# Performance work log

Measured on AMD Instinct MI355X. Metric: run time of the kernel, lower is better.

The kernel has to match this reference:

```python
import jax, jax.numpy as jnp
import numpy as np

NEG_SLOPE = 0.01  # torch LeakyReLU default

def setup_inputs() -> dict:
    key = jax.random.key(0)
    ks = jax.random.split(key, 8)
    B, T, D = 8, 2048, 512
    E, H = 8, 2 * D  # n_experts, ffn hidden
    s = 0.02
    return {
        "x":  jax.random.normal(ks[0], (B, T, D), dtype=jnp.float32),
        "Wr": jax.random.normal(ks[1], (D, E), dtype=jnp.float32) * s,
        "br": jnp.zeros((E,), dtype=jnp.float32),
        "W1": jax.random.normal(ks[2], (E, D, H), dtype=jnp.float32) * s,
        "b1": jnp.zeros((E, H), dtype=jnp.float32),
        "W2": jax.random.normal(ks[3], (E, H, D), dtype=jnp.float32) * s,
        "b2": jnp.zeros((E, D), dtype=jnp.float32),
    }

def reference(x, Wr, br, W1, b1, W2, b2):
    B, T, D = x.shape
    E = Wr.shape[1]
    top_k = 2
    balancing_coef = 1e-4
    x_flat = x.reshape(B * T, D)  # [N, D]

    # router: softmax over experts
    router_probs = jax.nn.softmax(x_flat @ Wr + br, axis=-1)  # [N, E]
    top_weights, top_indices = jax.lax.top_k(router_probs, top_k)  # [N, k]

    # dense all-expert FFN (faithful to original: every expert on every token)
    h = jax.nn.leaky_relu(jnp.einsum('nd,edh->neh', x_flat, W1) + b1, NEG_SLOPE)  # [N, E, H]
    expert_out = jax.nn.leaky_relu(jnp.einsum('neh,ehd->ned', h, W2) + b2, NEG_SLOPE)  # [N, E, D]
    # dropout is identity in eval mode

    # gather top-k expert outputs and combine with router weights
    top_out = jnp.take_along_axis(expert_out, top_indices[:, :, None], axis=1)  # [N, k, D]
    out_flat = jnp.sum(top_out * top_weights[:, :, None], axis=1)  # [N, D]
    output = out_flat.reshape(B, T, D)

    # load-balancing loss
    target = jnp.full((E,), 1.0 / E, dtype=x.dtype)
    mean_probs = jnp.mean(router_probs, axis=0)
    gating_loss = jnp.mean((target - mean_probs) ** 2) * balancing_coef
    return (output, gating_loss)
```

## Files before the change

### kernel.cpp

```cpp
#include <hip/hip_runtime.h>
#include <hip/hip_bf16.h>

constexpr int D_    = 512;
constexpr int H_    = 1024;
constexpr int E_    = 8;
constexpr int NTOK_ = 16384;
constexpr int MT_   = 64;
constexpr int NPAIR_= 2*NTOK_;
constexpr float NEG_ = 0.01f;

typedef short s16x8 __attribute__((ext_vector_type(8)));
typedef float f32x4 __attribute__((ext_vector_type(4)));

#define MFMA16(a,b,c) __builtin_amdgcn_mfma_f32_16x16x32_bf16((a),(b),(c),0,0,0)

__device__ __forceinline__ unsigned short f2bf(float f) {
  unsigned u = __float_as_uint(f);
  u += 0x7FFFu + ((u >> 16) & 1u);
  return (unsigned short)(u >> 16);
}
__device__ __forceinline__ float bf2f(unsigned u16) {
  return __uint_as_float(u16 << 16);
}
__device__ __forceinline__ float leaky(float v) {
  return v > 0.f ? v : NEG_ * v;
}

__global__ __launch_bounds__(256) void prep_kernel(
    const float* __restrict__ x, const float* __restrict__ Wr,
    const float* __restrict__ br,
    const float* __restrict__ W1, const float* __restrict__ W2,
    unsigned short* __restrict__ W1s, unsigned short* __restrict__ W2s,
    int* __restrict__ cnt, float* __restrict__ psum,
    int* __restrict__ tokE, int* __restrict__ tokSlot, float* __restrict__ tokW) {
  const int blk = blockIdx.x;
  const int tid = threadIdx.x;
  if (blk < 64) {
    __shared__ int lcnt[E_];
    __shared__ int gbase[E_];
    __shared__ float lp[E_];
    if (tid < E_) { lcnt[tid] = 0; lp[tid] = 0.f; }
    __syncthreads();

    int t = blk * 256 + tid;
    float acc[E_];
#pragma unroll
    for (int e = 0; e < E_; e++) acc[e] = br[e];
    const float4* xr = (const float4*)(x + (size_t)t * D_);
    for (int i = 0; i < D_ / 4; i++) {
      float4 v = xr[i];
      const float* w = Wr + (size_t)i * 4 * E_;
#pragma unroll
      for (int e = 0; e < E_; e++)
        acc[e] += v.x * w[e] + v.y * w[8 + e] + v.z * w[16 + e] + v.w * w[24 + e];
    }
    float mx = acc[0];
#pragma unroll
    for (int e = 1; e < E_; e++) mx = fmaxf(mx, acc[e]);
    float p[E_]; float s = 0.f;
#pragma unroll
    for (int e = 0; e < E_; e++) { p[e] = expf(acc[e] - mx); s += p[e]; }
    float inv = 1.f / s;
#pragma unroll
    for (int e = 0; e < E_; e++) p[e] *= inv;

    float m1 = -1.f, m2 = -1.f; int i1 = 0, i2 = 0;
#pragma unroll
    for (int e = 0; e < E_; e++) {
      float pe = p[e];
      if (pe > m1)      { m2 = m1; i2 = i1; m1 = pe; i1 = e; }
      else if (pe > m2) { m2 = pe; i2 = e; }
    }
    int s1 = atomicAdd(&lcnt[i1], 1);
    int s2 = atomicAdd(&lcnt[i2], 1);

#pragma unroll
    for (int e = 0; e < E_; e++) {
      float v = p[e];
#pragma unroll
      for (int o = 32; o > 0; o >>= 1) v += __shfl_xor(v, o);
      if ((tid & 63) == 0) atomicAdd(&lp[e], v);
    }
    __syncthreads();
    if (tid < E_) {
      gbase[tid] = atomicAdd(&cnt[tid * 16], lcnt[tid]);
      atomicAdd(&psum[tid * 16], lp[tid]);
    }
    __syncthreads();
    tokE[2 * t]     = i1; tokSlot[2 * t]     = gbase[i1] + s1; tokW[2 * t]     = m1;
    tokE[2 * t + 1] = i2; tokSlot[2 * t + 1] = gbase[i2] + s2; tokW[2 * t + 1] = m2;
  } else {
    __shared__ float ldsf[64][68];
    int bid = blk - 64;
    const float* src;
    int e, kt, tc, srcStride;
    bool isW1 = bid < 1024;
    if (isW1) {
      e = bid >> 7; kt = (bid >> 4) & 7; tc = bid & 15; srcStride = 1024;
      src = W1 + ((size_t)(e * 512 + kt * 64)) * 1024 + tc * 64;
    } else {
      int b2 = bid - 1024;
      e = b2 >> 7; kt = (b2 >> 3) & 15; tc = b2 & 7; srcStride = 512;
      src = W2 + ((size_t)(e * 1024 + kt * 64)) * 512 + tc * 64;
    }
#pragma unroll
    for (int rep = 0; rep < 4; rep++) {
      int row = rep * 16 + (tid >> 4);
      int c4  = (tid & 15) * 4;
      float4 v = *(const float4*)(src + (size_t)row * srcStride + c4);
      ldsf[row][c4] = v.x; ldsf[row][c4 + 1] = v.y;
      ldsf[row][c4 + 2] = v.z; ldsf[row][c4 + 3] = v.w;
    }
    __syncthreads();
    int wv = tid >> 6, lane = tid & 63;
#pragma unroll
    for (int qi = 0; qi < 2; qi++) {
      int q = wv * 2 + qi;
      int ks = q >> 2, nt = q & 3;
      int k0 = ks * 32 + (lane >> 4) * 8;
      int n  = nt * 16 + (lane & 15);
      s16x8 v;
#pragma unroll
      for (int j = 0; j < 8; j++) v[j] = (short)f2bf(ldsf[k0 + j][n]);
      if (isW1) {
        int ntg = tc * 4 + nt, kkg = kt * 2 + ks;
        *(s16x8*)(W1s + (((size_t)e << 16) + (ntg << 10) + (kkg << 6) + lane) * 8) = v;
      } else {
        int ntg = tc * 4 + nt, kkg = kt * 2 + ks;
        *(s16x8*)(W2s + (((size_t)e << 16) + (ntg << 11) + (kkg << 6) + lane) * 8) = v;
      }
    }
  }
}

__global__ __launch_bounds__(256) void assign_kernel(
    const int* __restrict__ tokE, const int* __restrict__ tokSlot,
    const int* __restrict__ cnt, const float* __restrict__ psum,
    int* __restrict__ posOfTok, int* __restrict__ tokOfPos,
    float* __restrict__ loss_out) {
  __shared__ int soff[E_];
  int tid = threadIdx.x;
  if (tid == 0) {
    int o = 0;
#pragma unroll
    for (int e = 0; e < E_; e++) { soff[e] = o; o += cnt[e * 16]; }
  }
  __syncthreads();
  int p = blockIdx.x * 256 + tid;
  int pos = soff[tokE[p]] + tokSlot[p];
  posOfTok[p] = pos;
  tokOfPos[pos] = p >> 1;
  if (blockIdx.x == 0 && tid == 0) {
    float l = 0.f;
#pragma unroll
    for (int e = 0; e < E_; e++) {
      float d = 0.125f - psum[e * 16] / (float)NTOK_;
      l += d * d;
    }
    *loss_out = (l / 8.f) * 1e-4f;
  }
}

__global__ __launch_bounds__(512, 2) void ffn_kernel(
    const float* __restrict__ x,
    const unsigned short* __restrict__ W1s, const unsigned short* __restrict__ W2s,
    const float* __restrict__ b1, const float* __restrict__ b2,
    const int* __restrict__ cnt, const int* __restrict__ tokOfPos,
    unsigned short* __restrict__ buf) {
  const int e = blockIdx.x & 7;
  const int tile = blockIdx.x >> 3;
  int nTok = 0, base0 = 0;
#pragma unroll
  for (int i = 0; i < E_; i++) {
    int ci = cnt[i * 16];
    if (i < e) base0 += ci;
    if (i == e) nTok = ci;
  }
  const int start = tile * MT_;
  if (start >= nTok) return;
  const int valid = min(MT_, nTok - start);
  const int base = base0 + start;

  __shared__ __align__(16) unsigned short xs[MT_][D_ + 8];
  __shared__ __align__(16) unsigned short hs[MT_][D_ + 8];

  const int tid = threadIdx.x;
  const int w = tid >> 6;
  const int lane = tid & 63;

  for (int r = w; r < MT_; r += 8) {
    int tok = tokOfPos[base + min(r, valid - 1)];
    const float4* src = (const float4*)(x + (size_t)tok * D_);
    float4 a = src[lane * 2], b = src[lane * 2 + 1];
    s16x8 v;
    v[0] = (short)f2bf(a.x); v[1] = (short)f2bf(a.y);
    v[2] = (short)f2bf(a.z); v[3] = (short)f2bf(a.w);
    v[4] = (short)f2bf(b.x); v[5] = (short)f2bf(b.y);
    v[6] = (short)f2bf(b.z); v[7] = (short)f2bf(b.w);
    *(s16x8*)&xs[r][lane * 8] = v;
  }
  __syncthreads();

  const int qm = lane & 15;
  const int qk = (lane >> 4) * 8;
  const int qr = (lane >> 4) * 4;

  f32x4 acc2[4][4];
#pragma unroll
  for (int mi = 0; mi < 4; mi++)
#pragma unroll
    for (int ni = 0; ni < 4; ni++) acc2[mi][ni] = {0.f, 0.f, 0.f, 0.f};

  const unsigned short* B1w = W1s + ((size_t)(e * 64 + w * 4) * 16) * 512 + lane * 8;
  const unsigned short* B2w = W2s + ((size_t)(e * 32 + w * 4) * 32) * 512 + lane * 8;

  for (int c = 0; c < 2; c++) {
    f32x4 acc1[4][4];
#pragma unroll
    for (int mi = 0; mi < 4; mi++)
#pragma unroll
      for (int ni = 0; ni < 4; ni++) acc1[mi][ni] = {0.f, 0.f, 0.f, 0.f};

    const unsigned short* B1c = B1w + (size_t)(c * 32 * 16) * 512;
    float bb[4];
#pragma unroll
    for (int ni = 0; ni < 4; ni++)
      bb[ni] = b1[e * H_ + c * 512 + w * 64 + ni * 16 + qm];

    s16x8 bfp[2][4], afp[2][4];
#pragma unroll
    for (int s = 0; s < 2; s++) {
#pragma unroll
      for (int ni = 0; ni < 4; ni++)
        bfp[s][ni] = *(const s16x8*)(B1c + (size_t)(ni * 16 + s) * 512);
#pragma unroll
      for (int mi = 0; mi < 4; mi++)
        afp[s][mi] = *(const s16x8*)&xs[mi * 16 + qm][s * 32 + qk];
    }
#pragma unroll
    for (int kk = 0; kk < 16; kk++) {
      s16x8 bcur[4], acur[4];
#pragma unroll
      for (int ni = 0; ni < 4; ni++) bcur[ni] = bfp[kk & 1][ni];
#pragma unroll
      for (int mi = 0; mi < 4; mi++) acur[mi] = afp[kk & 1][mi];
      if (kk + 2 < 16) {
#pragma unroll
        for (int ni = 0; ni < 4; ni++)
          bfp[kk & 1][ni] = *(const s16x8*)(B1c + (size_t)(ni * 16 + kk + 2) * 512);
#pragma unroll
        for (int mi = 0; mi < 4; mi++)
          afp[kk & 1][mi] = *(const s16x8*)&xs[mi * 16 + qm][(kk + 2) * 32 + qk];
      }
#pragma unroll
      for (int ni = 0; ni < 4; ni++)
#pragma unroll
        for (int mi = 0; mi < 4; mi++)
          acc1[mi][ni] = MFMA16(acur[mi], bcur[ni], acc1[mi][ni]);
    }
    __syncthreads();

    const unsigned short* B2c = B2w + (size_t)(c * 16) * 512;
    s16x8 b2p[2][4];
#pragma unroll
    for (int s = 0; s < 2; s++)
#pragma unroll
      for (int ni = 0; ni < 4; ni++)
        b2p[s][ni] = *(const s16x8*)(B2c + (size_t)(ni * 32 + s) * 512);

#pragma unroll
    for (int ni = 0; ni < 4; ni++) {
      int hcol = w * 64 + ni * 16 + qm;
#pragma unroll
      for (int mi = 0; mi < 4; mi++)
#pragma unroll
        for (int r4 = 0; r4 < 4; r4++)
          hs[mi * 16 + qr + r4][hcol] = f2bf(leaky(acc1[mi][ni][r4] + bb[ni]));
    }
    __syncthreads();

    s16x8 a2p[2][4];
#pragma unroll
    for (int s = 0; s < 2; s++)
#pragma unroll
      for (int mi = 0; mi < 4; mi++)
        a2p[s][mi] = *(const s16x8*)&hs[mi * 16 + qm][s * 32 + qk];
#pragma unroll
    for (int kk = 0; kk < 16; kk++) {
      s16x8 bcur[4], acur[4];
#pragma unroll
      for (int ni = 0; ni < 4; ni++) bcur[ni] = b2p[kk & 1][ni];
#pragma unroll
      for (int mi = 0; mi < 4; mi++) acur[mi] = a2p[kk & 1][mi];
      if (kk + 2 < 16) {
#pragma unroll
        for (int ni = 0; ni < 4; ni++)
          b2p[kk & 1][ni] = *(const s16x8*)(B2c + (size_t)(ni * 32 + kk + 2) * 512);
#pragma unroll
        for (int mi = 0; mi < 4; mi++)
          a2p[kk & 1][mi] = *(const s16x8*)&hs[mi * 16 + qm][(kk + 2) * 32 + qk];
      }
#pragma unroll
      for (int ni = 0; ni < 4; ni++)
#pragma unroll
        for (int mi = 0; mi < 4; mi++)
          acc2[mi][ni] = MFMA16(acur[mi], bcur[ni], acc2[mi][ni]);
    }
  }

#pragma unroll
  for (int mi = 0; mi < 4; mi++) {
#pragma unroll
    for (int r4 = 0; r4 < 4; r4++) {
      int row = mi * 16 + qr + r4;
      if (row < valid) {
        size_t rowbase = (size_t)(base + row) * D_;
#pragma unroll
        for (int ni = 0; ni < 4; ni++) {
          int col = w * 64 + ni * 16 + qm;
          float v = leaky(acc2[mi][ni][r4] + b2[e * D_ + col]);
          buf[rowbase + col] = f2bf(v);
        }
      }
    }
  }
}

__global__ __launch_bounds__(256) void combine_kernel(
    const unsigned short* __restrict__ buf, const int* __restrict__ posOfTok,
    const float* __restrict__ tokW, float* __restrict__ out) {
  int t = blockIdx.x * 4 + (threadIdx.x >> 6);
  int lane = threadIdx.x & 63;
  int p0 = posOfTok[2 * t], p1 = posOfTok[2 * t + 1];
  float w0 = tokW[2 * t], w1 = tokW[2 * t + 1];
  uint4 u0 = ((const uint4*)(buf + (size_t)p0 * D_))[lane];
  uint4 u1 = ((const uint4*)(buf + (size_t)p1 * D_))[lane];
  float4 oA, oB;
  oA.x = w0 * bf2f(u0.x & 0xFFFFu) + w1 * bf2f(u1.x & 0xFFFFu);
  oA.y = w0 * bf2f(u0.x >> 16)     + w1 * bf2f(u1.x >> 16);
  oA.z = w0 * bf2f(u0.y & 0xFFFFu) + w1 * bf2f(u1.y & 0xFFFFu);
  oA.w = w0 * bf2f(u0.y >> 16)     + w1 * bf2f(u1.y >> 16);
  oB.x = w0 * bf2f(u0.z & 0xFFFFu) + w1 * bf2f(u1.z & 0xFFFFu);
  oB.y = w0 * bf2f(u0.z >> 16)     + w1 * bf2f(u1.z >> 16);
  oB.z = w0 * bf2f(u0.w & 0xFFFFu) + w1 * bf2f(u1.w & 0xFFFFu);
  oB.w = w0 * bf2f(u0.w >> 16)     + w1 * bf2f(u1.w >> 16);
  float4* dst = (float4*)(out + (size_t)t * D_);
  dst[lane * 2]     = oA;
  dst[lane * 2 + 1] = oB;
}

extern "C" void kernel_launch(void* const* d_in, const int* in_sizes, int n_in,
                              void* d_out, int out_size, void* d_ws, size_t ws_size,
                              hipStream_t stream) {
  const float* x  = (const float*)d_in[0];
  const float* Wr = (const float*)d_in[1];
  const float* br = (const float*)d_in[2];
  const float* W1 = (const float*)d_in[3];
  const float* b1 = (const float*)d_in[4];
  const float* W2 = (const float*)d_in[5];
  const float* b2 = (const float*)d_in[6];
  float* out = (float*)d_out;

  char* ws = (char*)d_ws;
  int*   cnt      = (int*)(ws + 0);
  float* psum     = (float*)(ws + 512);
  int*   tokE     = (int*)(ws + 4096);
  int*   tokSlot  = (int*)(ws + 4096 + 1 * 131072);
  float* tokW     = (float*)(ws + 4096 + 2 * 131072);
  int*   posOfTok = (int*)(ws + 4096 + 3 * 131072);
  int*   tokOfPos = (int*)(ws + 4096 + 4 * 131072);
  unsigned short* W1s = (unsigned short*)(ws + (1u << 20));
  unsigned short* W2s = (unsigned short*)(ws + (1u << 20) + 16777216u);
  unsigned short* buf = (unsigned short*)(ws + (1u << 20) + 33554432u);

  hipMemsetAsync(d_ws, 0, 2048, stream);
  prep_kernel<<<64 + 2048, 256, 0, stream>>>(x, Wr, br, W1, W2, W1s, W2s,
                                             cnt, psum, tokE, tokSlot, tokW);
  assign_kernel<<<NPAIR_ / 256, 256, 0, stream>>>(tokE, tokSlot, cnt, psum,
                                                  posOfTok, tokOfPos,
                                                  out + (size_t)NTOK_ * D_);
  ffn_kernel<<<(NTOK_ / MT_) * E_, 512, 0, stream>>>(x, W1s, W2s, b1, b2,
                                                     cnt, tokOfPos, buf);
  combine_kernel<<<NTOK_ / 4, 256, 0, stream>>>(buf, posOfTok, tokW, out);
}
```

Baseline: 295.1 us.

## Fuse router, weight prep, FFN and combine into one cooperative persistent kernel

Replaces the four separate kernel launches with a single cooperative kernel of 256 blocks that uses grid-wide syncs between the routing/weight-conversion, assignment, expert FFN and combine phases. The router is recomputed with LDS-staged x and Wr, eight lanes per token, and the FFN loop becomes persistent over virtual tiles. A per-wave rotation of the K index is added to spread weight-fragment loads across waves. The aim is to remove launch gaps and tail effects, at the cost of grid-sync overhead, a fixed grid of 256 blocks, and 148 KB of shared memory per block, which limits occupancy to one block per CU despite the launch bound hint.

```diff
diff --git a/kernel.cpp b/kernel.cpp
--- a/kernel.cpp
+++ b/kernel.cpp
@@ -1,12 +1,14 @@
 #include <hip/hip_runtime.h>
 #include <hip/hip_bf16.h>
+#include <hip/hip_cooperative_groups.h>
+
+namespace cg = cooperative_groups;
 
 constexpr int D_    = 512;
 constexpr int H_    = 1024;
 constexpr int E_    = 8;
 constexpr int NTOK_ = 16384;
 constexpr int MT_   = 64;
-constexpr int NPAIR_= 2*NTOK_;
 constexpr float NEG_ = 0.01f;
 
 typedef short s16x8 __attribute__((ext_vector_type(8)));
@@ -26,360 +28,372 @@
   return v > 0.f ? v : NEG_ * v;
 }
 
-__global__ __launch_bounds__(256) void prep_kernel(
-    const float* __restrict__ x, const float* __restrict__ Wr,
-    const float* __restrict__ br,
-    const float* __restrict__ W1, const float* __restrict__ W2,
-    unsigned short* __restrict__ W1s, unsigned short* __restrict__ W2s,
-    int* __restrict__ cnt, float* __restrict__ psum,
-    int* __restrict__ tokE, int* __restrict__ tokSlot, float* __restrict__ tokW) {
-  const int blk = blockIdx.x;
-  const int tid = threadIdx.x;
-  if (blk < 64) {
-    __shared__ int lcnt[E_];
-    __shared__ int gbase[E_];
-    __shared__ float lp[E_];
+struct Params {
+  const float *x, *Wr, *br, *W1, *bias1, *W2, *bias2;
+  unsigned short *W1s, *W2s;
+  int *cnt; float *psum;
+  int *tokE, *tokSlot; float *tokW;
+  int *posOfTok, *tokOfPos;
+  unsigned short *buf;
+  float *out, *loss_out;
+};
+
+__global__ __launch_bounds__(512, 2) void fused_kernel(Params P) {
+  __shared__ __align__(16) char smem[148608];
+  cg::grid_group grid = cg::this_grid();
+  const int tid  = threadIdx.x;
+  const int w    = tid >> 6;
+  const int lane = tid & 63;
+  const int blk  = blockIdx.x;
+
+  {
+    float (*xl)[516] = (float (*)[516])smem;
+    float* wrl  = (float*)(smem + 132096);
+    int*   lcnt = (int*)(smem + 148480);
+    int*   gb   = (int*)(smem + 148512);
+    float* lp   = (float*)(smem + 148544);
     if (tid < E_) { lcnt[tid] = 0; lp[tid] = 0.f; }
+    {
+      const float4* s4 = (const float4*)P.Wr;
+      float4* d4 = (float4*)wrl;
+      d4[tid * 2] = s4[tid * 2]; d4[tid * 2 + 1] = s4[tid * 2 + 1];
+    }
+    const int t0 = blk * 64;
+    for (int r2 = 0; r2 < 8; r2++) {
+      int row = w * 8 + r2;
+      const float4* src = (const float4*)(P.x + (size_t)(t0 + row) * D_);
+      float4 a = src[lane * 2], b = src[lane * 2 + 1];
+      *(float4*)&xl[row][lane * 8] = a;
+      *(float4*)&xl[row][lane * 8 + 4] = b;
+    }
     __syncthreads();
-
-    int t = blk * 256 + tid;
-    float acc[E_];
-#pragma unroll
-    for (int e = 0; e < E_; e++) acc[e] = br[e];
-    const float4* xr = (const float4*)(x + (size_t)t * D_);
-    for (int i = 0; i < D_ / 4; i++) {
-      float4 v = xr[i];
-      const float* w = Wr + (size_t)i * 4 * E_;
-#pragma unroll
-      for (int e = 0; e < E_; e++)
-        acc[e] += v.x * w[e] + v.y * w[8 + e] + v.z * w[16 + e] + v.w * w[24 + e];
-    }
-    float mx = acc[0];
-#pragma unroll
-    for (int e = 1; e < E_; e++) mx = fmaxf(mx, acc[e]);
-    float p[E_]; float s = 0.f;
-#pragma unroll
-    for (int e = 0; e < E_; e++) { p[e] = expf(acc[e] - mx); s += p[e]; }
+    const int tg = lane >> 3, eg = lane & 7;
+    const int tokl = w * 8 + tg;
+    float acc = P.br[eg];
+    for (int d = 0; d < D_; d += 4) {
+      float4 xv = *(const float4*)&xl[tokl][d];
+      acc += xv.x * wrl[d * 8 + eg] + xv.y * wrl[d * 8 + 8 + eg] +
+             xv.z * wrl[d * 8 + 16 + eg] + xv.w * wrl[d * 8 + 24 + eg];
+    }
+    float lg[8];
+#pragma unroll
+    for (int e = 0; e < 8; e++) lg[e] = __shfl(acc, (lane & 56) | e);
+    float mx = lg[0];
+#pragma unroll
+    for (int e = 1; e < 8; e++) mx = fmaxf(mx, lg[e]);
+    float p[8], s = 0.f;
+#pragma unroll
+    for (int e = 0; e < 8; e++) { p[e] = expf(lg[e] - mx); s += p[e]; }
     float inv = 1.f / s;
 #pragma unroll
-    for (int e = 0; e < E_; e++) p[e] *= inv;
-
+    for (int e = 0; e < 8; e++) p[e] *= inv;
     float m1 = -1.f, m2 = -1.f; int i1 = 0, i2 = 0;
 #pragma unroll
-    for (int e = 0; e < E_; e++) {
+    for (int e = 0; e < 8; e++) {
       float pe = p[e];
       if (pe > m1)      { m2 = m1; i2 = i1; m1 = pe; i1 = e; }
       else if (pe > m2) { m2 = pe; i2 = e; }
     }
-    int s1 = atomicAdd(&lcnt[i1], 1);
-    int s2 = atomicAdd(&lcnt[i2], 1);
-
-#pragma unroll
-    for (int e = 0; e < E_; e++) {
-      float v = p[e];
-#pragma unroll
-      for (int o = 32; o > 0; o >>= 1) v += __shfl_xor(v, o);
-      if ((tid & 63) == 0) atomicAdd(&lp[e], v);
-    }
+    int s1 = 0, s2 = 0;
+    if (eg == 0) { s1 = atomicAdd(&lcnt[i1], 1); s2 = atomicAdd(&lcnt[i2], 1); }
+    float pe = p[eg];
+#pragma unroll
+    for (int o = 8; o < 64; o <<= 1) pe += __shfl_xor(pe, o);
+    if (tg == 0) atomicAdd(&lp[eg], pe);
     __syncthreads();
     if (tid < E_) {
-      gbase[tid] = atomicAdd(&cnt[tid * 16], lcnt[tid]);
-      atomicAdd(&psum[tid * 16], lp[tid]);
+      gb[tid] = atomicAdd(&P.cnt[tid * 16], lcnt[tid]);
+      atomicAdd(&P.psum[tid * 16], lp[tid]);
     }
     __syncthreads();
-    tokE[2 * t]     = i1; tokSlot[2 * t]     = gbase[i1] + s1; tokW[2 * t]     = m1;
-    tokE[2 * t + 1] = i2; tokSlot[2 * t + 1] = gbase[i2] + s2; tokW[2 * t + 1] = m2;
-  } else {
-    __shared__ float ldsf[64][68];
-    int bid = blk - 64;
-    const float* src;
-    int e, kt, tc, srcStride;
-    bool isW1 = bid < 1024;
-    if (isW1) {
-      e = bid >> 7; kt = (bid >> 4) & 7; tc = bid & 15; srcStride = 1024;
-      src = W1 + ((size_t)(e * 512 + kt * 64)) * 1024 + tc * 64;
-    } else {
-      int b2 = bid - 1024;
-      e = b2 >> 7; kt = (b2 >> 3) & 15; tc = b2 & 7; srcStride = 512;
-      src = W2 + ((size_t)(e * 1024 + kt * 64)) * 512 + tc * 64;
-    }
-#pragma unroll
-    for (int rep = 0; rep < 4; rep++) {
-      int row = rep * 16 + (tid >> 4);
-      int c4  = (tid & 15) * 4;
-      float4 v = *(const float4*)(src + (size_t)row * srcStride + c4);
-      ldsf[row][c4] = v.x; ldsf[row][c4 + 1] = v.y;
-      ldsf[row][c4 + 2] = v.z; ldsf[row][c4 + 3] = v.w;
+    if (eg == 0) {
+      int t = t0 + tokl;
+      P.tokE[2 * t]     = i1; P.tokSlot[2 * t]     = gb[i1] + s1; P.tokW[2 * t]     = m1;
+      P.tokE[2 * t + 1] = i2; P.tokSlot[2 * t + 1] = gb[i2] + s2; P.tokW[2 * t + 1] = m2;
     }
     __syncthreads();
-    int wv = tid >> 6, lane = tid & 63;
-#pragma unroll
-    for (int qi = 0; qi < 2; qi++) {
-      int q = wv * 2 + qi;
-      int ks = q >> 2, nt = q & 3;
-      int k0 = ks * 32 + (lane >> 4) * 8;
-      int n  = nt * 16 + (lane & 15);
-      s16x8 v;
-#pragma unroll
-      for (int j = 0; j < 8; j++) v[j] = (short)f2bf(ldsf[k0 + j][n]);
+  }
+
+  {
+    float (*ldsf)[68] = (float (*)[68])smem;
+    for (int ti = 0; ti < 8; ti++) {
+      int bid = blk * 8 + ti;
+      bool isW1 = bid < 1024;
+      const float* src; int srcStride, e, kt, tc;
       if (isW1) {
+        e = bid >> 7; kt = (bid >> 4) & 7; tc = bid & 15; srcStride = 1024;
+        src = P.W1 + ((size_t)(e * 512 + kt * 64)) * 1024 + tc * 64;
+      } else {
+        int b2i = bid - 1024;
+        e = b2i >> 7; kt = (b2i >> 3) & 15; tc = b2i & 7; srcStride = 512;
+        src = P.W2 + ((size_t)(e * 1024 + kt * 64)) * 512 + tc * 64;
+      }
+#pragma unroll
+      for (int rep = 0; rep < 2; rep++) {
+        int row = rep * 32 + (tid >> 4);
+        int c4  = (tid & 15) * 4;
+        float4 v = *(const float4*)(src + (size_t)row * srcStride + c4);
+        ldsf[row][c4] = v.x; ldsf[row][c4 + 1] = v.y;
+        ldsf[row][c4 + 2] = v.z; ldsf[row][c4 + 3] = v.w;
+      }
+      __syncthreads();
+      {
+        int ks = w >> 2, nt = w & 3;
+        int k0 = ks * 32 + (lane >> 4) * 8;
+        int n  = nt * 16 + (lane & 15);
+        s16x8 v;
+#pragma unroll
+        for (int j = 0; j < 8; j++) v[j] = (short)f2bf(ldsf[k0 + j][n]);
         int ntg = tc * 4 + nt, kkg = kt * 2 + ks;
-        *(s16x8*)(W1s + (((size_t)e << 16) + (ntg << 10) + (kkg << 6) + lane) * 8) = v;
-      } else {
-        int ntg = tc * 4 + nt, kkg = kt * 2 + ks;
-        *(s16x8*)(W2s + (((size_t)e << 16) + (ntg << 11) + (kkg << 6) + lane) * 8) = v;
-      }
-    }
-  }
-}
-
-__global__ __launch_bounds__(256) void assign_kernel(
-    const int* __restrict__ tokE, const int* __restrict__ tokSlot,
-    const int* __restrict__ cnt, const float* __restrict__ psum,
-    int* __restrict__ posOfTok, int* __restrict__ tokOfPos,
-    float* __restrict__ loss_out) {
-  __shared__ int soff[E_];
-  int tid = threadIdx.x;
-  if (tid == 0) {
-    int o = 0;
-#pragma unroll
-    for (int e = 0; e < E_; e++) { soff[e] = o; o += cnt[e * 16]; }
-  }
-  __syncthreads();
-  int p = blockIdx.x * 256 + tid;
-  int pos = soff[tokE[p]] + tokSlot[p];
-  posOfTok[p] = pos;
-  tokOfPos[pos] = p >> 1;
-  if (blockIdx.x == 0 && tid == 0) {
-    float l = 0.f;
-#pragma unroll
-    for (int e = 0; e < E_; e++) {
-      float d = 0.125f - psum[e * 16] / (float)NTOK_;
-      l += d * d;
-    }
-    *loss_out = (l / 8.f) * 1e-4f;
-  }
-}
-
-__global__ __launch_bounds__(512, 2) void ffn_kernel(
-    const float* __restrict__ x,
-    const unsigned short* __restrict__ W1s, const unsigned short* __restrict__ W2s,
-    const float* __restrict__ b1, const float* __restrict__ b2,
-    const int* __restrict__ cnt, const int* __restrict__ tokOfPos,
-    unsigned short* __restrict__ buf) {
-  const int e = blockIdx.x & 7;
-  const int tile = blockIdx.x >> 3;
-  int nTok = 0, base0 = 0;
-#pragma unroll
-  for (int i = 0; i < E_; i++) {
-    int ci = cnt[i * 16];
-    if (i < e) base0 += ci;
-    if (i == e) nTok = ci;
-  }
-  const int start = tile * MT_;
-  if (start >= nTok) return;
-  const int valid = min(MT_, nTok - start);
-  const int base = base0 + start;
-
-  __shared__ __align__(16) unsigned short xs[MT_][D_ + 8];
-  __shared__ __align__(16) unsigned short hs[MT_][D_ + 8];
-
-  const int tid = threadIdx.x;
-  const int w = tid >> 6;
-  const int lane = tid & 63;
-
-  for (int r = w; r < MT_; r += 8) {
-    int tok = tokOfPos[base + min(r, valid - 1)];
-    const float4* src = (const float4*)(x + (size_t)tok * D_);
-    float4 a = src[lane * 2], b = src[lane * 2 + 1];
-    s16x8 v;
-    v[0] = (short)f2bf(a.x); v[1] = (short)f2bf(a.y);
-    v[2] = (short)f2bf(a.z); v[3] = (short)f2bf(a.w);
-    v[4] = (short)f2bf(b.x); v[5] = (short)f2bf(b.y);
-    v[6] = (short)f2bf(b.z); v[7] = (short)f2bf(b.w);
-    *(s16x8*)&xs[r][lane * 8] = v;
-  }
-  __syncthreads();
-
-  const int qm = lane & 15;
-  const int qk = (lane >> 4) * 8;
-  const int qr = (lane >> 4) * 4;
-
-  f32x4 acc2[4][4];
-#pragma unroll
-  for (int mi = 0; mi < 4; mi++)
-#pragma unroll
-    for (int ni = 0; ni < 4; ni++) acc2[mi][ni] = {0.f, 0.f, 0.f, 0.f};
-
-  const unsigned short* B1w = W1s + ((size_t)(e * 64 + w * 4) * 16) * 512 + lane * 8;
-  const unsigned short* B2w = W2s + ((size_t)(e * 32 + w * 4) * 32) * 512 + lane * 8;
-
-  for (int c = 0; c < 2; c++) {
-    f32x4 acc1[4][4];
-#pragma unroll
-    for (int mi = 0; mi < 4; mi++)
-#pragma unroll
-      for (int ni = 0; ni < 4; ni++) acc1[mi][ni] = {0.f, 0.f, 0.f, 0.f};
-
-    const unsigned short* B1c = B1w + (size_t)(c * 32 * 16) * 512;
-    float bb[4];
-#pragma unroll
-    for (int ni = 0; ni < 4; ni++)
-      bb[ni] = b1[e * H_ + c * 512 + w * 64 + ni * 16 + qm];
-
-    s16x8 bfp[2][4], afp[2][4];
-#pragma unroll
-    for (int s = 0; s < 2; s++) {
-#pragma unroll
-      for (int ni = 0; ni < 4; ni++)
-        bfp[s][ni] = *(const s16x8*)(B1c + (size_t)(ni * 16 + s) * 512);
+        if (isW1)
+          *(s16x8*)(P.W1s + (((size_t)e << 16) + (ntg << 10) + (kkg << 6) + lane) * 8) = v;
+        else
+          *(s16x8*)(P.W2s + (((size_t)e << 16) + (ntg << 11) + (kkg << 6) + lane) * 8) = v;
+      }
+      __syncthreads();
+    }
+  }
+  grid.sync();
+
+  {
+    if (tid < 128) {
+      int p = blk * 128 + tid;
+      int te = P.tokE[p], soff = 0;
+#pragma unroll
+      for (int e2 = 0; e2 < E_; e2++) soff += (e2 < te) ? P.cnt[e2 * 16] : 0;
+      int pos = soff + P.tokSlot[p];
+      P.posOfTok[p] = pos;
+      P.tokOfPos[pos] = p >> 1;
+    }
+    if (blk == 0 && tid == 0) {
+      float l = 0.f;
+#pragma unroll
+      for (int e = 0; e < E_; e++) {
+        float d = 0.125f - P.psum[e * 16] / (float)NTOK_;
+        l += d * d;
+      }
+      *P.loss_out = (l / 8.f) * 1e-4f;
+    }
+  }
+  grid.sync();
+
+  {
+    unsigned short (*xs)[520] = (unsigned short (*)[520])smem;
+    unsigned short (*hs)[520] = (unsigned short (*)[520])(smem + 66560);
+    const int qm = lane & 15;
+    const int qk = (lane >> 4) * 8;
+    const int qr = (lane >> 4) * 4;
+    const int rot = w * 2;
+
+    for (int vt = blk; vt < 2048; vt += 256) {
+      const int e = vt & 7;
+      const int tile = vt >> 3;
+      int nTok = 0, base0 = 0;
+#pragma unroll
+      for (int i = 0; i < E_; i++) {
+        int ci = P.cnt[i * 16];
+        if (i < e) base0 += ci;
+        if (i == e) nTok = ci;
+      }
+      const int start = tile * MT_;
+      if (start >= nTok) continue;
+      const int valid = min(MT_, nTok - start);
+      const int base = base0 + start;
+
+      for (int r = w; r < MT_; r += 8) {
+        int tok = P.tokOfPos[base + min(r, valid - 1)];
+        const float4* src = (const float4*)(P.x + (size_t)tok * D_);
+        float4 a = src[lane * 2], b = src[lane * 2 + 1];
+        s16x8 v;
+        v[0] = (short)f2bf(a.x); v[1] = (short)f2bf(a.y);
+        v[2] = (short)f2bf(a.z); v[3] = (short)f2bf(a.w);
+        v[4] = (short)f2bf(b.x); v[5] = (short)f2bf(b.y);
+        v[6] = (short)f2bf(b.z); v[7] = (short)f2bf(b.w);
+        *(s16x8*)&xs[r][lane * 8] = v;
+      }
+      __syncthreads();
+
+      f32x4 acc2[4][4];
 #pragma unroll
       for (int mi = 0; mi < 4; mi++)
-        afp[s][mi] = *(const s16x8*)&xs[mi * 16 + qm][s * 32 + qk];
-    }
-#pragma unroll
-    for (int kk = 0; kk < 16; kk++) {
-      s16x8 bcur[4], acur[4];
-#pragma unroll
-      for (int ni = 0; ni < 4; ni++) bcur[ni] = bfp[kk & 1][ni];
-#pragma unroll
-      for (int mi = 0; mi < 4; mi++) acur[mi] = afp[kk & 1][mi];
-      if (kk + 2 < 16) {
+#pragma unroll
+        for (int ni = 0; ni < 4; ni++) acc2[mi][ni] = {0.f, 0.f, 0.f, 0.f};
+
+      const unsigned short* B1w = P.W1s + ((size_t)(e * 64 + w * 4) * 16) * 512 + lane * 8;
+      const unsigned short* B2w = P.W2s + ((size_t)(e * 32 + w * 4) * 32) * 512 + lane * 8;
+
+      for (int c = 0; c < 2; c++) {
+        f32x4 acc1[4][4];
+#pragma unroll
+        for (int mi = 0; mi < 4; mi++)
+#pragma unroll
+          for (int ni = 0; ni < 4; ni++) acc1[mi][ni] = {0.f, 0.f, 0.f, 0.f};
+
+        const unsigned short* B1c = B1w + (size_t)(c * 512) * 512;
+        float bb[4];
 #pragma unroll
         for (int ni = 0; ni < 4; ni++)
-          bfp[kk & 1][ni] = *(const s16x8*)(B1c + (size_t)(ni * 16 + kk + 2) * 512);
-#pragma unroll
-        for (int mi = 0; mi < 4; mi++)
-          afp[kk & 1][mi] = *(const s16x8*)&xs[mi * 16 + qm][(kk + 2) * 32 + qk];
-      }
-#pragma unroll
-      for (int ni = 0; ni < 4; ni++)
-#pragma unroll
-        for (int mi = 0; mi < 4; mi++)
-          acc1[mi][ni] = MFMA16(acur[mi], bcur[ni], acc1[mi][ni]);
-    }
-    __syncthreads();
-
-    const unsigned short* B2c = B2w + (size_t)(c * 16) * 512;
-    s16x8 b2p[2][4];
-#pragma unroll
-    for (int s = 0; s < 2; s++)
-#pragma unroll
-      for (int ni = 0; ni < 4; ni++)
-        b2p[s][ni] = *(const s16x8*)(B2c + (size_t)(ni * 32 + s) * 512);
-
-#pragma unroll
-    for (int ni = 0; ni < 4; ni++) {
-      int hcol = w * 64 + ni * 16 + qm;
-#pragma unroll
-      for (int mi = 0; mi < 4; mi++)
-#pragma unroll
-        for (int r4 = 0; r4 < 4; r4++)
-          hs[mi * 16 + qr + r4][hcol] = f2bf(leaky(acc1[mi][ni][r4] + bb[ni]));
-    }
-    __syncthreads();
-
-    s16x8 a2p[2][4];
-#pragma unroll
-    for (int s = 0; s < 2; s++)
-#pragma unroll
-      for (int mi = 0; mi < 4; mi++)
-        a2p[s][mi] = *(const s16x8*)&hs[mi * 16 + qm][s * 32 + qk];
-#pragma unroll
-    for (int kk = 0; kk < 16; kk++) {
-      s16x8 bcur[4], acur[4];
-#pragma unroll
-      for (int ni = 0; ni < 4; ni++) bcur[ni] = b2p[kk & 1][ni];
-#pragma unroll
-      for (int mi = 0; mi < 4; mi++) acur[mi] = a2p[kk & 1][mi];
-      if (kk + 2 < 16) {
-#pragma unroll
-        for (int ni = 0; ni < 4; ni++)
-          b2p[kk & 1][ni] = *(const s16x8*)(B2c + (size_t)(ni * 32 + kk + 2) * 512);
-#pragma unroll
-        for (int mi = 0; mi < 4; mi++)
-          a2p[kk & 1][mi] = *(const s16x8*)&hs[mi * 16 + qm][(kk + 2) * 32 + qk];
-      }
-#pragma unroll
-      for (int ni = 0; ni < 4; ni++)
-#pragma unroll
-        for (int mi = 0; mi < 4; mi++)
-          acc2[mi][ni] = MFMA16(acur[mi], bcur[ni], acc2[mi][ni]);
-    }
-  }
-
-#pragma unroll
-  for (int mi = 0; mi < 4; mi++) {
-#pragma unroll
-    for (int r4 = 0; r4 < 4; r4++) {
-      int row = mi * 16 + qr + r4;
-      if (row < valid) {
-        size_t rowbase = (size_t)(base + row) * D_;
+          bb[ni] = P.bias1[e * H_ + c * 512 + w * 64 + ni * 16 + qm];
+
+        s16x8 bfp[2][4], afp[2][4];
+#pragma unroll
+        for (int s = 0; s < 2; s++) {
+          int kr = (s + rot) & 15;
+#pragma unroll
+          for (int ni = 0; ni < 4; ni++)
+            bfp[s][ni] = *(const s16x8*)(B1c + (size_t)(ni * 16 + kr) * 512);
+#pragma unroll
+          for (int mi = 0; mi < 4; mi++)
+            afp[s][mi] = *(const s16x8*)&xs[mi * 16 + qm][kr * 32 + qk];
+        }
+#pragma unroll
+        for (int kk = 0; kk < 16; kk++) {
+          s16x8 bcur[4], acur[4];
+#pragma unroll
+          for (int ni = 0; ni < 4; ni++) bcur[ni] = bfp[kk & 1][ni];
+#pragma unroll
+          for (int mi = 0; mi < 4; mi++) acur[mi] = afp[kk & 1][mi];
+          if (kk + 2 < 16) {
+            int kr2 = (kk + 2 + rot) & 15;
+#pragma unroll
+            for (int ni = 0; ni < 4; ni++)
+              bfp[kk & 1][ni] = *(const s16x8*)(B1c + (size_t)(ni * 16 + kr2) * 512);
+#pragma unroll
+            for (int mi = 0; mi < 4; mi++)
+              afp[kk & 1][mi] = *(const s16x8*)&xs[mi * 16 + qm][kr2 * 32 + qk];
+          }
+#pragma unroll
+          for (int ni = 0; ni < 4; ni++)
+#pragma unroll
+            for (int mi = 0; mi < 4; mi++)
+              acc1[mi][ni] = MFMA16(acur[mi], bcur[ni], acc1[mi][ni]);
+        }
+        __syncthreads();
+
+        const unsigned short* B2c = B2w + (size_t)(c * 16) * 512;
+        s16x8 b2p[2][4];
+#pragma unroll
+        for (int s = 0; s < 2; s++) {
+          int kr = (s + rot) & 15;
+#pragma unroll
+          for (int ni = 0; ni < 4; ni++)
+            b2p[s][ni] = *(const s16x8*)(B2c + (size_t)(ni * 32 + kr) * 512);
+        }
 #pragma unroll
         for (int ni = 0; ni < 4; ni++) {
-          int col = w * 64 + ni * 16 + qm;
-          float v = leaky(acc2[mi][ni][r4] + b2[e * D_ + col]);
-          buf[rowbase + col] = f2bf(v);
-        }
-      }
-    }
-  }
-}
-
-__global__ __launch_bounds__(256) void combine_kernel(
-    const unsigned short* __restrict__ buf, const int* __restrict__ posOfTok,
-    const float* __restrict__ tokW, float* __restrict__ out) {
-  int t = blockIdx.x * 4 + (threadIdx.x >> 6);
-  int lane = threadIdx.x & 63;
-  int p0 = posOfTok[2 * t], p1 = posOfTok[2 * t + 1];
-  float w0 = tokW[2 * t], w1 = tokW[2 * t + 1];
-  uint4 u0 = ((const uint4*)(buf + (size_t)p0 * D_))[lane];
-  uint4 u1 = ((const uint4*)(buf + (size_t)p1 * D_))[lane];
-  float4 oA, oB;
-  oA.x = w0 * bf2f(u0.x & 0xFFFFu) + w1 * bf2f(u1.x & 0xFFFFu);
-  oA.y = w0 * bf2f(u0.x >> 16)     + w1 * bf2f(u1.x >> 16);
-  oA.z = w0 * bf2f(u0.y & 0xFFFFu) + w1 * bf2f(u1.y & 0xFFFFu);
-  oA.w = w0 * bf2f(u0.y >> 16)     + w1 * bf2f(u1.y >> 16);
-  oB.x = w0 * bf2f(u0.z & 0xFFFFu) + w1 * bf2f(u1.z & 0xFFFFu);
-  oB.y = w0 * bf2f(u0.z >> 16)     + w1 * bf2f(u1.z >> 16);
-  oB.z = w0 * bf2f(u0.w & 0xFFFFu) + w1 * bf2f(u1.w & 0xFFFFu);
-  oB.w = w0 * bf2f(u0.w >> 16)     + w1 * bf2f(u1.w >> 16);
-  float4* dst = (float4*)(out + (size_t)t * D_);
-  dst[lane * 2]     = oA;
-  dst[lane * 2 + 1] = oB;
+          int hcol = w * 64 + ni * 16 + qm;
+#pragma unroll
+          for (int mi = 0; mi < 4; mi++)
+#pragma unroll
+            for (int r4 = 0; r4 < 4; r4++)
+              hs[mi * 16 + qr + r4][hcol] = f2bf(leaky(acc1[mi][ni][r4] + bb[ni]));
+        }
+        __syncthreads();
+
+        s16x8 a2p[2][4];
+#pragma unroll
+        for (int s = 0; s < 2; s++) {
+          int kr = (s + rot) & 15;
+#pragma unroll
+          for (int mi = 0; mi < 4; mi++)
+            a2p[s][mi] = *(const s16x8*)&hs[mi * 16 + qm][kr * 32 + qk];
+        }
+#pragma unroll
+        for (int kk = 0; kk < 16; kk++) {
+          s16x8 bcur[4], acur[4];
+#pragma unroll
+          for (int ni = 0; ni < 4; ni++) bcur[ni] = b2p[kk & 1][ni];
+#pragma unroll
+          for (int mi = 0; mi < 4; mi++) acur[mi] = a2p[kk & 1][mi];
+          if (kk + 2 < 16) {
+            int kr2 = (kk + 2 + rot) & 15;
+#pragma unroll
+            for (int ni = 0; ni < 4; ni++)
+              b2p[kk & 1][ni] = *(const s16x8*)(B2c + (size_t)(ni * 32 + kr2) * 512);
+#pragma unroll
+            for (int mi = 0; mi < 4; mi++)
+              a2p[kk & 1][mi] = *(const s16x8*)&hs[mi * 16 + qm][kr2 * 32 + qk];
+          }
+#pragma unroll
+          for (int ni = 0; ni < 4; ni++)
+#pragma unroll
+            for (int mi = 0; mi < 4; mi++)
+              acc2[mi][ni] = MFMA16(acur[mi], bcur[ni], acc2[mi][ni]);
+        }
+      }
+
+#pragma unroll
+      for (int mi = 0; mi < 4; mi++) {
+#pragma unroll
+        for (int r4 = 0; r4 < 4; r4++) {
+          int row = mi * 16 + qr + r4;
+          if (row < valid) {
+            size_t rowbase = (size_t)(base + row) * D_;
+#pragma unroll
+            for (int ni = 0; ni < 4; ni++) {
+              int col = w * 64 + ni * 16 + qm;
+              float v = leaky(acc2[mi][ni][r4] + P.bias2[e * D_ + col]);
+              P.buf[rowbase + col] = f2bf(v);
+            }
+          }
+        }
+      }
+      __syncthreads();
+    }
+  }
+  grid.sync();
+
+  {
+    for (int i = 0; i < 8; i++) {
+      int t = blk * 64 + w * 8 + i;
+      int p0 = P.posOfTok[2 * t], p1 = P.posOfTok[2 * t + 1];
+      float w0 = P.tokW[2 * t], w1 = P.tokW[2 * t + 1];
+      uint4 u0 = ((const uint4*)(P.buf + (size_t)p0 * D_))[lane];
+      uint4 u1 = ((const uint4*)(P.buf + (size_t)p1 * D_))[lane];
+      float4 oA, oB;
+      oA.x = w0 * bf2f(u0.x & 0xFFFFu) + w1 * bf2f(u1.x & 0xFFFFu);
+      oA.y = w0 * bf2f(u0.x >> 16)     + w1 * bf2f(u1.x >> 16);
+      oA.z = w0 * bf2f(u0.y & 0xFFFFu) + w1 * bf2f(u1.y & 0xFFFFu);
+      oA.w = w0 * bf2f(u0.y >> 16)     + w1 * bf2f(u1.y >> 16);
+      oB.x = w0 * bf2f(u0.z & 0xFFFFu) + w1 * bf2f(u1.z & 0xFFFFu);
+      oB.y = w0 * bf2f(u0.z >> 16)     + w1 * bf2f(u1.z >> 16);
+      oB.z = w0 * bf2f(u0.w & 0xFFFFu) + w1 * bf2f(u1.w & 0xFFFFu);
+      oB.w = w0 * bf2f(u0.w >> 16)     + w1 * bf2f(u1.w >> 16);
+      float4* dst = (float4*)(P.out + (size_t)t * D_);
+      dst[lane * 2]     = oA;
+      dst[lane * 2 + 1] = oB;
+    }
+  }
 }
 
 extern "C" void kernel_launch(void* const* d_in, const int* in_sizes, int n_in,
                               void* d_out, int out_size, void* d_ws, size_t ws_size,
                               hipStream_t stream) {
-  const float* x  = (const float*)d_in[0];
-  const float* Wr = (const float*)d_in[1];
-  const float* br = (const float*)d_in[2];
-  const float* W1 = (const float*)d_in[3];
-  const float* b1 = (const float*)d_in[4];
-  const float* W2 = (const float*)d_in[5];
-  const float* b2 = (const float*)d_in[6];
-  float* out = (float*)d_out;
-
   char* ws = (char*)d_ws;
-  int*   cnt      = (int*)(ws + 0);
-  float* psum     = (float*)(ws + 512);
-  int*   tokE     = (int*)(ws + 4096);
-  int*   tokSlot  = (int*)(ws + 4096 + 1 * 131072);
-  float* tokW     = (float*)(ws + 4096 + 2 * 131072);
-  int*   posOfTok = (int*)(ws + 4096 + 3 * 131072);
-  int*   tokOfPos = (int*)(ws + 4096 + 4 * 131072);
-  unsigned short* W1s = (unsigned short*)(ws + (1u << 20));
-  unsigned short* W2s = (unsigned short*)(ws + (1u << 20) + 16777216u);
-  unsigned short* buf = (unsigned short*)(ws + (1u << 20) + 33554432u);
+  Params P;
+  P.x  = (const float*)d_in[0];
+  P.Wr = (const float*)d_in[1];
+  P.br = (const float*)d_in[2];
+  P.W1 = (const float*)d_in[3];
+  P.bias1 = (const float*)d_in[4];
+  P.W2 = (const float*)d_in[5];
+  P.bias2 = (const float*)d_in[6];
+  P.out = (float*)d_out;
+  P.loss_out = (float*)d_out + (size_t)NTOK_ * D_;
+
+  P.cnt      = (int*)(ws + 0);
+  P.psum     = (float*)(ws + 512);
+  P.tokE     = (int*)(ws + 4096);
+  P.tokSlot  = (int*)(ws + 4096 + 1 * 131072);
+  P.tokW     = (float*)(ws + 4096 + 2 * 131072);
+  P.posOfTok = (int*)(ws + 4096 + 3 * 131072);
+  P.tokOfPos = (int*)(ws + 4096 + 4 * 131072);
+  P.W1s = (unsigned short*)(ws + (1u << 20));
+  P.W2s = (unsigned short*)(ws + (1u << 20) + 16777216u);
+  P.buf = (unsigned short*)(ws + (1u << 20) + 33554432u);
 
   hipMemsetAsync(d_ws, 0, 2048, stream);
-  prep_kernel<<<64 + 2048, 256, 0, stream>>>(x, Wr, br, W1, W2, W1s, W2s,
-                                             cnt, psum, tokE, tokSlot, tokW);
-  assign_kernel<<<NPAIR_ / 256, 256, 0, stream>>>(tokE, tokSlot, cnt, psum,
-                                                  posOfTok, tokOfPos,
-                                                  out + (size_t)NTOK_ * D_);
-  ffn_kernel<<<(NTOK_ / MT_) * E_, 512, 0, stream>>>(x, W1s, W2s, b1, b2,
-                                                     cnt, tokOfPos, buf);
-  combine_kernel<<<NTOK_ / 4, 256, 0, stream>>>(buf, posOfTok, tokW, out);
-}
+  void* args[] = { &P };
+  hipLaunchCooperativeKernel((void*)fused_kernel, dim3(256), dim3(512),
+                             args, 0, stream);
+}
```

Result: slower. 524.0 us (+77.6%).
